# Performance work log

Hardware: AMD Instinct MI355X
Metric: run time of the kernel (lower is better)

## Reference

```python
import jax, jax.numpy as jnp
import numpy as np

RES = 32  # voxel resolution (init_kwargs)


def setup_inputs() -> dict:
    key = jax.random.key(0)
    k1, k2 = jax.random.split(key)
    B, C, N = 8, 64, 100000
    features = jax.random.normal(k1, (B, C, N), dtype=jnp.float32)
    coords = jax.random.normal(k2, (B, 3, N), dtype=jnp.float32)
    return {"features": features, "coords": coords}


def reference(features, coords):
    # features: [B, C, N], coords: [B, 3, N]
    R = RES
    B, C, N = features.shape
    coords = jax.lax.stop_gradient(coords)  # coords.detach()

    # normalize: center, scale by 2*max point radius, shift to [0,1]
    norm_coords = coords - jnp.mean(coords, axis=2, keepdims=True)
    radius = jnp.linalg.norm(norm_coords, axis=1, keepdims=True)      # [B,1,N]
    scale = jnp.max(radius, axis=2, keepdims=True) * 2.0               # [B,1,1]
    norm_coords = norm_coords / scale + 0.5
    norm_coords = jnp.clip(norm_coords * R, 0, R - 1)                  # [B,3,N]

    vox = jnp.round(norm_coords).astype(jnp.int32)                     # [B,3,N]
    flat = (vox[:, 0] * R + vox[:, 1]) * R + vox[:, 2]                 # [B,N]
    idx = (flat + jnp.arange(B, dtype=jnp.int32)[:, None] * (R * R * R)).reshape(-1)

    feats = features.transpose(0, 2, 1).reshape(B * N, C)              # [B*N, C]
    sums = jax.ops.segment_sum(feats, idx, num_segments=B * R * R * R)
    cnts = jax.ops.segment_sum(jnp.ones((B * N,), features.dtype), idx,
                               num_segments=B * R * R * R)
    avg = sums / jnp.maximum(cnts, 1.0)[:, None]                       # avg voxelize
    grid = avg.reshape(B, R, R, R, C).transpose(0, 4, 1, 2, 3)         # [B,C,R,R,R]
    return grid, norm_coords
```

## Files before the change

kernel.cpp:

```cpp
#include <hip/hip_runtime.h>
#include <hip/hip_bf16.h>

#define RESV 32
#define R3V (RESV * RESV * RESV)
#define R3P1 (R3V + 1)
#define CH 64

__device__ __forceinline__ unsigned short f2bf(float f) {
    __hip_bfloat16 h = __float2bfloat16(f);
    unsigned short u;
    __builtin_memcpy(&u, &h, 2);
    return u;
}
__device__ __forceinline__ unsigned int pkbf(float lo, float hi) {
    return (unsigned int)f2bf(lo) | ((unsigned int)f2bf(hi) << 16);
}
__device__ __forceinline__ float blo(unsigned int u) { return __uint_as_float(u << 16); }
__device__ __forceinline__ float bhi(unsigned int u) { return __uint_as_float(u & 0xffff0000u); }


__global__ void k_zero(float4* __restrict__ p, int n4) {
    const int i = blockIdx.x * blockDim.x + threadIdx.x;
    if (i < n4) p[i] = make_float4(0.f, 0.f, 0.f, 0.f);
}

__global__ void k_sums(const float* __restrict__ coords, float* __restrict__ ws_sums, int N) {
    const int b = blockIdx.y;
    const float* cb = coords + (size_t)b * 3 * N;
    float sx = 0.f, sy = 0.f, sz = 0.f;
    for (int n = blockIdx.x * blockDim.x + threadIdx.x; n < N; n += gridDim.x * blockDim.x) {
        sx += cb[n];
        sy += cb[N + n];
        sz += cb[2 * N + n];
    }
    for (int off = 32; off > 0; off >>= 1) {
        sx += __shfl_down(sx, off);
        sy += __shfl_down(sy, off);
        sz += __shfl_down(sz, off);
    }
    __shared__ float red[3][4];
    const int lane = threadIdx.x & 63;
    const int wv   = threadIdx.x >> 6;
    if (lane == 0) { red[0][wv] = sx; red[1][wv] = sy; red[2][wv] = sz; }
    __syncthreads();
    if (threadIdx.x == 0) {
        float tx = 0.f, ty = 0.f, tz = 0.f;
        const int nw = blockDim.x >> 6;
        for (int w = 0; w < nw; ++w) { tx += red[0][w]; ty += red[1][w]; tz += red[2][w]; }
        atomicAdd(&ws_sums[b * 3 + 0], tx);
        atomicAdd(&ws_sums[b * 3 + 1], ty);
        atomicAdd(&ws_sums[b * 3 + 2], tz);
    }
}

__global__ void k_maxrad(const float* __restrict__ coords, const float* __restrict__ ws_sums,
                         unsigned int* __restrict__ ws_max, int N) {
    const int b = blockIdx.y;
    const float invN = 1.0f / (float)N;
    const float mx = ws_sums[b * 3 + 0] * invN;
    const float my = ws_sums[b * 3 + 1] * invN;
    const float mz = ws_sums[b * 3 + 2] * invN;
    const float* cb = coords + (size_t)b * 3 * N;
    float r = 0.f;
    for (int n = blockIdx.x * blockDim.x + threadIdx.x; n < N; n += gridDim.x * blockDim.x) {
        const float dx = cb[n] - mx;
        const float dy = cb[N + n] - my;
        const float dz = cb[2 * N + n] - mz;
        r = fmaxf(r, sqrtf(dx * dx + dy * dy + dz * dz));
    }
    for (int off = 32; off > 0; off >>= 1) r = fmaxf(r, __shfl_down(r, off));
    __shared__ float red[4];
    const int lane = threadIdx.x & 63;
    const int wv   = threadIdx.x >> 6;
    if (lane == 0) red[wv] = r;
    __syncthreads();
    if (threadIdx.x == 0) {
        const int nw = blockDim.x >> 6;
        float t = 0.f;
        for (int w = 0; w < nw; ++w) t = fmaxf(t, red[w]);
        atomicMax(&ws_max[b], __float_as_uint(t));
    }
}

__global__ void k_points(const float* __restrict__ coords, const float* __restrict__ ws_sums,
                         const unsigned int* __restrict__ ws_max,
                         float* __restrict__ norm_out, int* __restrict__ idx_ws,
                         int* __restrict__ jloc, int* __restrict__ counts, int N) {
    const int b = blockIdx.y;
    const int n = blockIdx.x * blockDim.x + threadIdx.x;
    if (n >= N) return;
    const float invN  = 1.0f / (float)N;
    const float scale = 2.0f * __uint_as_float(ws_max[b]);
    const float* cb = coords + (size_t)b * 3 * N;
    float* nb = norm_out + (size_t)b * 3 * N;

    int flat = 0;
#pragma unroll
    for (int d = 0; d < 3; ++d) {
        const float mean = ws_sums[b * 3 + d] * invN;
        float nc = (cb[d * N + n] - mean) / scale + 0.5f;
        nc = fminf(fmaxf(nc * (float)RESV, 0.0f), (float)(RESV - 1));
        nb[d * N + n] = nc;
        flat = flat * RESV + (int)rintf(nc);
    }
    idx_ws[(size_t)b * N + n] = flat;
    jloc[(size_t)b * N + n] = atomicAdd(&counts[b * R3V + flat], 1);
}

__global__ __launch_bounds__(1024, 1) void k_scan(const int* __restrict__ counts,
                                                  int* __restrict__ start, int N) {
    const int b = blockIdx.x;
    const int t = threadIdx.x;
    const int base  = b * R3V + t * 32;
    const int baseS = b * R3P1 + t * 32;
    int c[32];
    int T = 0;
#pragma unroll
    for (int i = 0; i < 32; ++i) { c[i] = counts[base + i]; T += c[i]; }
    int incl = T;
    const int lane = t & 63;
    for (int off = 1; off < 64; off <<= 1) {
        int y = __shfl_up(incl, off);
        if (lane >= off) incl += y;
    }
    __shared__ int wsum[16];
    __shared__ int wbase[16];
    const int w = t >> 6;
    if (lane == 63) wsum[w] = incl;
    __syncthreads();
    if (t == 0) {
        int run = 0;
        for (int i = 0; i < 16; ++i) { wbase[i] = run; run += wsum[i]; }
    }
    __syncthreads();
    int run = wbase[w] + incl - T;
#pragma unroll
    for (int i = 0; i < 32; ++i) {
        start[baseS + i] = run;
        run += c[i];
    }
    if (t == 1023) start[b * R3P1 + R3V] = run;
}

__global__ __launch_bounds__(1024, 2) void k_transpose_perm(
        const float* __restrict__ feats, const int* __restrict__ idx_ws,
        const int* __restrict__ jloc, const int* __restrict__ startv,
        unsigned int* __restrict__ fTs32, int* __restrict__ voxid, int N) {
    __shared__ unsigned short tile[256][66];
    __shared__ int jrow[256];
    const int b  = blockIdx.y;
    const int n0 = blockIdx.x * 256;
    const int t  = threadIdx.x;
    const float* fb = feats + (size_t)b * 64 * N;

    const int c = t >> 4;
    const int q = t & 15;
    if (n0 + 256 <= N) {
#pragma unroll
        for (int i = 0; i < 4; ++i) {
            const int nn = q * 4 + i * 64;
            const float4 f = *(const float4*)(fb + (size_t)c * N + n0 + nn);
            tile[nn + 0][c] = f2bf(f.x);
            tile[nn + 1][c] = f2bf(f.y);
            tile[nn + 2][c] = f2bf(f.z);
            tile[nn + 3][c] = f2bf(f.w);
        }
    } else {
        for (int i = 0; i < 4; ++i) {
            const int nn = q * 4 + i * 64;
            for (int u = 0; u < 4; ++u) {
                const int n = n0 + nn + u;
                tile[nn + u][c] = f2bf((n < N) ? fb[(size_t)c * N + n] : 0.f);
            }
        }
    }
    if (t < 256) {
        const int n = n0 + t;
        if (n < N) {
            const int v = idx_ws[(size_t)b * N + n];
            const int j = startv[(size_t)b * R3P1 + v] + jloc[(size_t)b * N + n];
            jrow[t] = j;
            voxid[(size_t)b * N + j] = v;
        }
    }
    __syncthreads();

    const int wv   = t >> 6;
    const int lane = t & 63;
    const int lc   = lane & 31;
    const int ph   = lane >> 5;
    unsigned int* fo = fTs32 + (size_t)b * N * 32;
#pragma unroll
    for (int k = 0; k < 8; ++k) {
        const int p = k * 32 + wv * 2 + ph;
        if (n0 + p < N) {
            const unsigned int d = *(const unsigned int*)&tile[p][2 * lc];
            fo[(size_t)jrow[p] * 32 + lc] = d;
        }
    }
}

__global__ __launch_bounds__(256) void k_gather4(const unsigned int* __restrict__ fTs32,
                                                 const int* __restrict__ voxid,
                                                 const int* __restrict__ startv,
                                                 unsigned int* __restrict__ gridT2,
                                                 int N, int nchunk) {
    const int w     = threadIdx.x >> 6;
    const int lane  = threadIdx.x & 63;
    const int p     = lane >> 4;
    const int lc    = lane & 15;
    const int chunk = blockIdx.x * 4 + w;
    if (chunk >= nchunk) return;
    const int b    = blockIdx.y;
    const int c0   = chunk * CH;
    const int end0 = min(c0 + CH, N);
    const uint2* fb = (const uint2*)(fTs32 + (size_t)b * N * 32);
    const int* vi = voxid  + (size_t)b * N;
    const int* sv = startv + (size_t)b * R3P1;
    uint2* gT = (uint2*)(gridT2) + (size_t)b * R3V * 16;

    int j;
    {
        const int v = vi[c0];
        const int s = sv[v];
        j = (s < c0) ? sv[v + 1] : s;
    }
    while (j < end0) {
        const int v = vi[j];
        const int e = sv[v + 1];
        float a0 = 0.f, a1 = 0.f, a2 = 0.f, a3 = 0.f;
        int r = j + p;
        for (; r + 12 < e; r += 16) {
            const uint2 u0 = fb[(size_t)(r + 0) * 16 + lc];
            const uint2 u1 = fb[(size_t)(r + 4) * 16 + lc];
            const uint2 u2 = fb[(size_t)(r + 8) * 16 + lc];
            const uint2 u3 = fb[(size_t)(r + 12) * 16 + lc];
            a0 += (blo(u0.x) + blo(u1.x)) + (blo(u2.x) + blo(u3.x));
            a1 += (bhi(u0.x) + bhi(u1.x)) + (bhi(u2.x) + bhi(u3.x));
            a2 += (blo(u0.y) + blo(u1.y)) + (blo(u2.y) + blo(u3.y));
            a3 += (bhi(u0.y) + bhi(u1.y)) + (bhi(u2.y) + bhi(u3.y));
        }
        for (; r < e; r += 4) {
            const uint2 u = fb[(size_t)r * 16 + lc];
            a0 += blo(u.x);
            a1 += bhi(u.x);
            a2 += blo(u.y);
            a3 += bhi(u.y);
        }
        a0 += __shfl_xor(a0, 16); a0 += __shfl_xor(a0, 32);
        a1 += __shfl_xor(a1, 16); a1 += __shfl_xor(a1, 32);
        a2 += __shfl_xor(a2, 16); a2 += __shfl_xor(a2, 32);
        a3 += __shfl_xor(a3, 16); a3 += __shfl_xor(a3, 32);
        if (p == 0) {
            gT[(size_t)v * 16 + lc] = make_uint2(pkbf(a0, a1), pkbf(a2, a3));
        }
        j = e;
    }
}

__global__ __launch_bounds__(256) void k_fin(const unsigned int* __restrict__ gridT2,
                                             const int* __restrict__ counts,
                                             float* __restrict__ grid) {
    __shared__ float tile[64][65];
    const int b    = blockIdx.y;
    const int v0   = blockIdx.x * 64;
    const int t    = threadIdx.x;
    const int lane = t & 63;
    const int w    = t >> 6;
    const unsigned int* g = gridT2 + ((size_t)b * R3V + v0) * 32;
#pragma unroll
    for (int k = 0; k < 8; ++k) {
        const int i  = t + k * 256;
        const int v  = i >> 5;
        const int cd = i & 31;
        const unsigned int u = g[i];
        tile[v][2 * cd]     = blo(u);
        tile[v][2 * cd + 1] = bhi(u);
    }
    __syncthreads();
    const int cnt  = counts[(size_t)b * R3V + v0 + lane];
    const float rc = 1.0f / fmaxf((float)cnt, 1.0f);
    const bool occ = cnt > 0;
    float* gb = grid + (size_t)b * 64 * R3V;
#pragma unroll
    for (int k = 0; k < 16; ++k) {
        const int c = w + k * 4;
        gb[(size_t)c * R3V + v0 + lane] = occ ? tile[lane][c] * rc : 0.0f;
    }
}


__device__ __forceinline__ int swz(int v) {
    return v ^ ((v >> 5) & 31) ^ ((v >> 10) & 31);
}

__global__ void k_recip_fb(const int* __restrict__ cnt, float* __restrict__ recip, int total) {
    const int i = blockIdx.x * blockDim.x + threadIdx.x;
    if (i < total) recip[i] = 1.0f / fmaxf((float)cnt[i], 1.0f);
}

__global__ __launch_bounds__(1024, 1) void k_scatter_lds(
        const float* __restrict__ feats, const int* __restrict__ idx_ws,
        const float* __restrict__ recip, float* __restrict__ grid, int N, int C) {
    extern __shared__ float acc[];
    const int bc  = blockIdx.x;
    const int b   = bc / C;
    const int tid = threadIdx.x;
    for (int i = tid * 4; i < R3V; i += blockDim.x * 4)
        *(float4*)(acc + i) = make_float4(0.f, 0.f, 0.f, 0.f);
    __syncthreads();
    const float* fb = feats  + (size_t)bc * N;
    const int*   ib = idx_ws + (size_t)b  * N;
    const int n4 = (N / 4) * 4;
    for (int n = tid * 4; n < n4; n += blockDim.x * 4) {
        const float4 f = *(const float4*)(fb + n);
        const int4  ix = *(const int4*)(ib + n);
        atomicAdd(&acc[swz(ix.x)], f.x);
        atomicAdd(&acc[swz(ix.y)], f.y);
        atomicAdd(&acc[swz(ix.z)], f.z);
        atomicAdd(&acc[swz(ix.w)], f.w);
    }
    for (int n = n4 + tid; n < N; n += blockDim.x) atomicAdd(&acc[swz(ib[n])], fb[n]);
    __syncthreads();
    const float* rb = recip + (size_t)b * R3V;
    float*       gb = grid  + (size_t)bc * R3V;
    for (int i = tid; i < R3V; i += blockDim.x)
        gb[i] = acc[swz(i)] * rb[i];
}


extern "C" void kernel_launch(void* const* d_in, const int* in_sizes, int n_in,
                              void* d_out, int out_size, void* d_ws, size_t ws_size,
                              hipStream_t stream) {
    const float* feats  = (const float*)d_in[0];
    const float* coords = (const float*)d_in[1];

    const long long s0 = in_sizes[0], s1 = in_sizes[1];
    const int BC = (int)(((long long)out_size - s1) / R3V);
    const int N  = (int)(s0 / BC);
    const int B  = (int)(s1 / (3LL * N));
    const int C  = BC / B;

    float* out_grid = (float*)d_out;
    float* out_norm = out_grid + (size_t)BC * R3V;

    const size_t BR3 = (size_t)B * R3V;
    const size_t BN  = (size_t)B * N;
    const size_t o_counts = 64;
    const size_t o_start  = o_counts + BR3;
    const size_t o_recip  = o_start + (size_t)B * R3P1;
    const size_t o_idx    = o_recip + BR3;
    const size_t o_jloc   = o_idx + BN;
    const size_t o_voxid  = o_jloc + BN;
    size_t o_gridT = (o_voxid + BN + 63) & ~(size_t)63;
    size_t o_fTs   = (o_gridT + BR3 * 32 + 63) & ~(size_t)63;
    const size_t need = (o_fTs + BN * 32) * sizeof(float);

    float*        ws_sums = (float*)d_ws;
    unsigned int* ws_max  = (unsigned int*)((float*)d_ws + 32);
    int*          counts  = (int*)d_ws + o_counts;
    int*          startv  = (int*)d_ws + o_start;
    float*        recip   = (float*)d_ws + o_recip;
    int*          idx_ws  = (int*)d_ws + o_idx;
    int*          jloc    = (int*)d_ws + o_jloc;
    int*          voxid   = (int*)d_ws + o_voxid;
    unsigned int* gridT2  = (unsigned int*)((float*)d_ws + o_gridT);
    unsigned int* fTs32   = (unsigned int*)((float*)d_ws + o_fTs);

    const int zero4 = (int)((64 + BR3) / 4);
    k_zero<<<(zero4 + 255) / 256, 256, 0, stream>>>((float4*)d_ws, zero4);

    const int BLK = 256;
    dim3 gRed(32, B);
    k_sums<<<gRed, BLK, 0, stream>>>(coords, ws_sums, N);
    k_maxrad<<<gRed, BLK, 0, stream>>>(coords, ws_sums, ws_max, N);

    dim3 gPts((N + BLK - 1) / BLK, B);
    k_points<<<gPts, BLK, 0, stream>>>(coords, ws_sums, ws_max, out_norm, idx_ws, jloc, counts, N);

    if (ws_size >= need && C == 64) {
        k_scan<<<dim3(B), 1024, 0, stream>>>(counts, startv, N);
        dim3 gT((N + 255) / 256, B);
        k_transpose_perm<<<gT, 1024, 0, stream>>>(feats, idx_ws, jloc, startv,
                                                  fTs32, voxid, N);
        const int nchunk = (N + CH - 1) / CH;
        dim3 gG((nchunk + 3) / 4, B);
        k_gather4<<<gG, 256, 0, stream>>>(fTs32, voxid, startv, gridT2, N, nchunk);
        dim3 gF(R3V / 64, B);
        k_fin<<<gF, 256, 0, stream>>>(gridT2, counts, out_grid);
    } else {
        const int tot = B * R3V;
        k_recip_fb<<<(tot + BLK - 1) / BLK, BLK, 0, stream>>>(counts, recip, tot);
        k_scatter_lds<<<dim3(BC), 1024, R3V * sizeof(float), stream>>>(
            feats, idx_ws, recip, out_grid, N, C);
    }
}
```

Baseline: 231.0 us.

## Fold zeroing into reduction, pack voxel index and slot, interleave batches in grids

Removes the separate zero kernel by having k_sums clear the counts buffer. The float atomics for sums and max are replaced with per-block partials that later kernels reduce in shared memory. Voxel index and per-voxel slot are packed into one 32-bit word, cutting a buffer and a load. The transpose and gather grids are flattened so batches interleave across blocks, and the gather chunk size doubles. Risks: the counts zeroing relies on the grid exactly covering B*R3V/4 int4s (true for 32 blocks x 256 threads x 4 per batch), and the 17-bit slot field limits points per voxel.

```diff
diff --git a/kernel.cpp b/kernel.cpp
--- a/kernel.cpp
+++ b/kernel.cpp
@@ -4,7 +4,7 @@
 #define RESV 32
 #define R3V (RESV * RESV * RESV)
 #define R3P1 (R3V + 1)
-#define CH 64
+#define CH 128
 
 __device__ __forceinline__ unsigned short f2bf(float f) {
     __hip_bfloat16 h = __float2bfloat16(f);
@@ -19,13 +19,13 @@
 __device__ __forceinline__ float bhi(unsigned int u) { return __uint_as_float(u & 0xffff0000u); }
 
 
-__global__ void k_zero(float4* __restrict__ p, int n4) {
-    const int i = blockIdx.x * blockDim.x + threadIdx.x;
-    if (i < n4) p[i] = make_float4(0.f, 0.f, 0.f, 0.f);
-}
-
-__global__ void k_sums(const float* __restrict__ coords, float* __restrict__ ws_sums, int N) {
+__global__ void k_sums(const float* __restrict__ coords, float* __restrict__ part,
+                       int4* __restrict__ counts4, int N) {
     const int b = blockIdx.y;
+    {
+        const int g = (blockIdx.y * gridDim.x + blockIdx.x) * blockDim.x + threadIdx.x;
+        counts4[g] = make_int4(0, 0, 0, 0);
+    }
     const float* cb = coords + (size_t)b * 3 * N;
     float sx = 0.f, sy = 0.f, sz = 0.f;
     for (int n = blockIdx.x * blockDim.x + threadIdx.x; n < N; n += gridDim.x * blockDim.x) {
@@ -47,19 +47,22 @@
         float tx = 0.f, ty = 0.f, tz = 0.f;
         const int nw = blockDim.x >> 6;
         for (int w = 0; w < nw; ++w) { tx += red[0][w]; ty += red[1][w]; tz += red[2][w]; }
-        atomicAdd(&ws_sums[b * 3 + 0], tx);
-        atomicAdd(&ws_sums[b * 3 + 1], ty);
-        atomicAdd(&ws_sums[b * 3 + 2], tz);
-    }
-}
-
-__global__ void k_maxrad(const float* __restrict__ coords, const float* __restrict__ ws_sums,
-                         unsigned int* __restrict__ ws_max, int N) {
+        float* p = part + (b * 32 + blockIdx.x) * 3;
+        p[0] = tx; p[1] = ty; p[2] = tz;
+    }
+}
+
+__global__ void k_maxrad(const float* __restrict__ coords, const float* __restrict__ part,
+                         float* __restrict__ maxp, int N) {
     const int b = blockIdx.y;
+    __shared__ float sp[96];
+    if (threadIdx.x < 96) sp[threadIdx.x] = part[b * 96 + threadIdx.x];
+    __syncthreads();
     const float invN = 1.0f / (float)N;
-    const float mx = ws_sums[b * 3 + 0] * invN;
-    const float my = ws_sums[b * 3 + 1] * invN;
-    const float mz = ws_sums[b * 3 + 2] * invN;
+    float mx = 0.f, my = 0.f, mz = 0.f;
+    for (int x = 0; x < 32; ++x) { mx += sp[x * 3]; my += sp[x * 3 + 1]; mz += sp[x * 3 + 2]; }
+    mx *= invN; my *= invN; mz *= invN;
+
     const float* cb = coords + (size_t)b * 3 * N;
     float r = 0.f;
     for (int n = blockIdx.x * blockDim.x + threadIdx.x; n < N; n += gridDim.x * blockDim.x) {
@@ -78,33 +81,44 @@
         const int nw = blockDim.x >> 6;
         float t = 0.f;
         for (int w = 0; w < nw; ++w) t = fmaxf(t, red[w]);
-        atomicMax(&ws_max[b], __float_as_uint(t));
-    }
-}
-
-__global__ void k_points(const float* __restrict__ coords, const float* __restrict__ ws_sums,
-                         const unsigned int* __restrict__ ws_max,
-                         float* __restrict__ norm_out, int* __restrict__ idx_ws,
-                         int* __restrict__ jloc, int* __restrict__ counts, int N) {
+        maxp[b * 32 + blockIdx.x] = t;
+    }
+}
+
+__global__ void k_points(const float* __restrict__ coords, const float* __restrict__ part,
+                         const float* __restrict__ maxp,
+                         float* __restrict__ norm_out, unsigned int* __restrict__ pk,
+                         int* __restrict__ counts, int N) {
     const int b = blockIdx.y;
+    __shared__ float sp[96];
+    __shared__ float mp[32];
+    if (threadIdx.x < 96) sp[threadIdx.x] = part[b * 96 + threadIdx.x];
+    if (threadIdx.x < 32) mp[threadIdx.x] = maxp[b * 32 + threadIdx.x];
+    __syncthreads();
+    const float invN = 1.0f / (float)N;
+    float mean[3] = {0.f, 0.f, 0.f};
+    float mrad = 0.f;
+    for (int x = 0; x < 32; ++x) {
+        mean[0] += sp[x * 3]; mean[1] += sp[x * 3 + 1]; mean[2] += sp[x * 3 + 2];
+        mrad = fmaxf(mrad, mp[x]);
+    }
+    const float scale = 2.0f * mrad;
+
     const int n = blockIdx.x * blockDim.x + threadIdx.x;
     if (n >= N) return;
-    const float invN  = 1.0f / (float)N;
-    const float scale = 2.0f * __uint_as_float(ws_max[b]);
     const float* cb = coords + (size_t)b * 3 * N;
     float* nb = norm_out + (size_t)b * 3 * N;
 
     int flat = 0;
 #pragma unroll
     for (int d = 0; d < 3; ++d) {
-        const float mean = ws_sums[b * 3 + d] * invN;
-        float nc = (cb[d * N + n] - mean) / scale + 0.5f;
+        float nc = (cb[d * N + n] - mean[d] * invN) / scale + 0.5f;
         nc = fminf(fmaxf(nc * (float)RESV, 0.0f), (float)(RESV - 1));
         nb[d * N + n] = nc;
         flat = flat * RESV + (int)rintf(nc);
     }
-    idx_ws[(size_t)b * N + n] = flat;
-    jloc[(size_t)b * N + n] = atomicAdd(&counts[b * R3V + flat], 1);
+    const int jl = atomicAdd(&counts[b * R3V + flat], 1);
+    pk[(size_t)b * N + n] = ((unsigned int)flat << 17) | (unsigned int)jl;
 }
 
 __global__ __launch_bounds__(1024, 1) void k_scan(const int* __restrict__ counts,
@@ -143,14 +157,15 @@
 }
 
 __global__ __launch_bounds__(1024, 2) void k_transpose_perm(
-        const float* __restrict__ feats, const int* __restrict__ idx_ws,
-        const int* __restrict__ jloc, const int* __restrict__ startv,
-        unsigned int* __restrict__ fTs32, int* __restrict__ voxid, int N) {
+        const float* __restrict__ feats, const unsigned int* __restrict__ pk,
+        const int* __restrict__ startv,
+        unsigned int* __restrict__ fTs32, int* __restrict__ voxid, int N, int B) {
     __shared__ unsigned short tile[256][66];
     __shared__ int jrow[256];
-    const int b  = blockIdx.y;
-    const int n0 = blockIdx.x * 256;
-    const int t  = threadIdx.x;
+    const int bid = blockIdx.x;
+    const int b   = bid % B;
+    const int n0  = (bid / B) * 256;
+    const int t   = threadIdx.x;
     const float* fb = feats + (size_t)b * 64 * N;
 
     const int c = t >> 4;
@@ -177,8 +192,9 @@
     if (t < 256) {
         const int n = n0 + t;
         if (n < N) {
-            const int v = idx_ws[(size_t)b * N + n];
-            const int j = startv[(size_t)b * R3P1 + v] + jloc[(size_t)b * N + n];
+            const unsigned int p = pk[(size_t)b * N + n];
+            const int v  = (int)(p >> 17);
+            const int j  = startv[(size_t)b * R3P1 + v] + (int)(p & 0x1FFFFu);
             jrow[t] = j;
             voxid[(size_t)b * N + j] = v;
         }
@@ -204,14 +220,15 @@
                                                  const int* __restrict__ voxid,
                                                  const int* __restrict__ startv,
                                                  unsigned int* __restrict__ gridT2,
-                                                 int N, int nchunk) {
+                                                 int N, int nchunk, int B) {
+    const int bid   = blockIdx.x;
+    const int b     = bid % B;
     const int w     = threadIdx.x >> 6;
     const int lane  = threadIdx.x & 63;
     const int p     = lane >> 4;
     const int lc    = lane & 15;
-    const int chunk = blockIdx.x * 4 + w;
+    const int chunk = (bid / B) * 4 + w;
     if (chunk >= nchunk) return;
-    const int b    = blockIdx.y;
     const int c0   = chunk * CH;
     const int end0 = min(c0 + CH, N);
     const uint2* fb = (const uint2*)(fTs32 + (size_t)b * N * 32);
@@ -300,7 +317,7 @@
 }
 
 __global__ __launch_bounds__(1024, 1) void k_scatter_lds(
-        const float* __restrict__ feats, const int* __restrict__ idx_ws,
+        const float* __restrict__ feats, const unsigned int* __restrict__ pk,
         const float* __restrict__ recip, float* __restrict__ grid, int N, int C) {
     extern __shared__ float acc[];
     const int bc  = blockIdx.x;
@@ -309,18 +326,9 @@
     for (int i = tid * 4; i < R3V; i += blockDim.x * 4)
         *(float4*)(acc + i) = make_float4(0.f, 0.f, 0.f, 0.f);
     __syncthreads();
-    const float* fb = feats  + (size_t)bc * N;
-    const int*   ib = idx_ws + (size_t)b  * N;
-    const int n4 = (N / 4) * 4;
-    for (int n = tid * 4; n < n4; n += blockDim.x * 4) {
-        const float4 f = *(const float4*)(fb + n);
-        const int4  ix = *(const int4*)(ib + n);
-        atomicAdd(&acc[swz(ix.x)], f.x);
-        atomicAdd(&acc[swz(ix.y)], f.y);
-        atomicAdd(&acc[swz(ix.z)], f.z);
-        atomicAdd(&acc[swz(ix.w)], f.w);
-    }
-    for (int n = n4 + tid; n < N; n += blockDim.x) atomicAdd(&acc[swz(ib[n])], fb[n]);
+    const float* fb = feats + (size_t)bc * N;
+    const unsigned int* ib = pk + (size_t)b * N;
+    for (int n = tid; n < N; n += blockDim.x) atomicAdd(&acc[swz((int)(ib[n] >> 17))], fb[n]);
     __syncthreads();
     const float* rb = recip + (size_t)b * R3V;
     float*       gb = grid  + (size_t)bc * R3V;
@@ -346,52 +354,48 @@
 
     const size_t BR3 = (size_t)B * R3V;
     const size_t BN  = (size_t)B * N;
-    const size_t o_counts = 64;
+    const size_t o_counts = 1024;
     const size_t o_start  = o_counts + BR3;
     const size_t o_recip  = o_start + (size_t)B * R3P1;
-    const size_t o_idx    = o_recip + BR3;
-    const size_t o_jloc   = o_idx + BN;
-    const size_t o_voxid  = o_jloc + BN;
+    const size_t o_pk     = o_recip + BR3;
+    const size_t o_voxid  = o_pk + BN;
     size_t o_gridT = (o_voxid + BN + 63) & ~(size_t)63;
     size_t o_fTs   = (o_gridT + BR3 * 32 + 63) & ~(size_t)63;
     const size_t need = (o_fTs + BN * 32) * sizeof(float);
 
-    float*        ws_sums = (float*)d_ws;
-    unsigned int* ws_max  = (unsigned int*)((float*)d_ws + 32);
+    float*        ws_part = (float*)d_ws;
+    float*        ws_maxp = (float*)d_ws + 768;
     int*          counts  = (int*)d_ws + o_counts;
     int*          startv  = (int*)d_ws + o_start;
     float*        recip   = (float*)d_ws + o_recip;
-    int*          idx_ws  = (int*)d_ws + o_idx;
-    int*          jloc    = (int*)d_ws + o_jloc;
+    unsigned int* pk      = (unsigned int*)d_ws + o_pk;
     int*          voxid   = (int*)d_ws + o_voxid;
     unsigned int* gridT2  = (unsigned int*)((float*)d_ws + o_gridT);
     unsigned int* fTs32   = (unsigned int*)((float*)d_ws + o_fTs);
 
-    const int zero4 = (int)((64 + BR3) / 4);
-    k_zero<<<(zero4 + 255) / 256, 256, 0, stream>>>((float4*)d_ws, zero4);
-
     const int BLK = 256;
     dim3 gRed(32, B);
-    k_sums<<<gRed, BLK, 0, stream>>>(coords, ws_sums, N);
-    k_maxrad<<<gRed, BLK, 0, stream>>>(coords, ws_sums, ws_max, N);
+    k_sums<<<gRed, BLK, 0, stream>>>(coords, ws_part, (int4*)counts, N);
+    k_maxrad<<<gRed, BLK, 0, stream>>>(coords, ws_part, ws_maxp, N);
 
     dim3 gPts((N + BLK - 1) / BLK, B);
-    k_points<<<gPts, BLK, 0, stream>>>(coords, ws_sums, ws_max, out_norm, idx_ws, jloc, counts, N);
+    k_points<<<gPts, BLK, 0, stream>>>(coords, ws_part, ws_maxp, out_norm, pk, counts, N);
 
     if (ws_size >= need && C == 64) {
         k_scan<<<dim3(B), 1024, 0, stream>>>(counts, startv, N);
-        dim3 gT((N + 255) / 256, B);
-        k_transpose_perm<<<gT, 1024, 0, stream>>>(feats, idx_ws, jloc, startv,
-                                                  fTs32, voxid, N);
+        const int nTB = (N + 255) / 256;
+        k_transpose_perm<<<dim3(nTB * B), 1024, 0, stream>>>(feats, pk, startv,
+                                                             fTs32, voxid, N, B);
         const int nchunk = (N + CH - 1) / CH;
-        dim3 gG((nchunk + 3) / 4, B);
-        k_gather4<<<gG, 256, 0, stream>>>(fTs32, voxid, startv, gridT2, N, nchunk);
+        const int nGB = (nchunk + 3) / 4;
+        k_gather4<<<dim3(nGB * B), 256, 0, stream>>>(fTs32, voxid, startv, gridT2,
+                                                     N, nchunk, B);
         dim3 gF(R3V / 64, B);
         k_fin<<<gF, 256, 0, stream>>>(gridT2, counts, out_grid);
     } else {
         const int tot = B * R3V;
         k_recip_fb<<<(tot + BLK - 1) / BLK, BLK, 0, stream>>>(counts, recip, tot);
         k_scatter_lds<<<dim3(BC), 1024, R3V * sizeof(float), stream>>>(
-            feats, idx_ws, recip, out_grid, N, C);
-    }
-}
+            feats, pk, recip, out_grid, N, C);
+    }
+}
```

New measurement: 261.3 us. +13.1%, slower.
